# Kernel optimization log

Measured on AMD Instinct MI355X. Metric: run time of the kernel, lower is better.

Reference implementation:

```python
import jax, jax.numpy as jnp
import numpy as np

B, S, D = 4, 2048, 1024
H, HD = 16, 64
WINDOW = 128


def setup_inputs() -> dict:
    key = jax.random.key(0)
    ks = jax.random.split(key, 8)
    scale = 1.0 / np.sqrt(D)
    return {
        "hidden_states": jax.random.normal(ks[0], (B, S, D), dtype=jnp.float32),
        "attention_mask": jnp.zeros((B, 1, 1, S), dtype=jnp.float32),
        "Wq": jax.random.normal(ks[1], (D, D), dtype=jnp.float32) * scale,
        "bq": jnp.zeros((D,), dtype=jnp.float32),
        "Wk": jax.random.normal(ks[2], (D, D), dtype=jnp.float32) * scale,
        "bk": jnp.zeros((D,), dtype=jnp.float32),
        "Wv": jax.random.normal(ks[3], (D, D), dtype=jnp.float32) * scale,
        "bv": jnp.zeros((D,), dtype=jnp.float32),
    }


def _proj(x, W, b):
    # [b t D] -> [b h t d]
    p = x @ W.T + b
    return p.reshape(x.shape[0], x.shape[1], H, HD).transpose(0, 2, 1, 3)


def reference(hidden_states, attention_mask, Wq, bq, Wk, bk, Wv, bv):
    q = _proj(hidden_states, Wq, bq)  # [b h t d]
    k = _proj(hidden_states, Wk, bk)
    v = _proj(hidden_states, Wv, bv)

    scores = jnp.einsum("bhtd,bhsd->bhts", q, k) / np.sqrt(HD)  # [b h t s]
    pos = jnp.arange(S)
    i, j = pos[:, None], pos[None, :]
    # causal (j <= i) AND sliding window (i - j <= w)
    allowed = (j <= i) & ((i - j) <= WINDOW)  # [t s]
    scores = jnp.where(allowed[None, None], scores, -jnp.inf)
    scores = scores + attention_mask  # additive padding mask [b,1,1,s]
    probs = jax.nn.softmax(scores, axis=-1)  # dropout identity in eval
    ctx = jnp.einsum("bhts,bhsd->bhtd", probs, v)
    return ctx.transpose(0, 2, 1, 3).reshape(B, S, D)
```

## Files before the change

### kernel.cpp

```cpp
#include <hip/hip_runtime.h>
#include <cstdint>

#define BDIM 4
#define SEQ 2048
#define DMODEL 1024
#define NH 16
#define HDIM 64

typedef __attribute__((ext_vector_type(8))) short bf16x8;
typedef __attribute__((ext_vector_type(4))) float f32x4;
typedef __attribute__((ext_vector_type(4))) int i32x4;
typedef __attribute__((ext_vector_type(4))) unsigned short u16x4;

#define MFMA16(a, b, c) __builtin_amdgcn_mfma_f32_16x16x32_bf16(a, b, c, 0, 0, 0)

__device__ __forceinline__ unsigned short f2bf(float x) {
    unsigned int u = __float_as_uint(x);
    unsigned int r = (u + 0x7FFFu + ((u >> 16) & 1u)) >> 16;
    return (unsigned short)r;
}

__device__ __forceinline__ void gload16(const void* g, void* l) {
    __builtin_amdgcn_global_load_lds(
        (const __attribute__((address_space(1))) unsigned int*)g,
        (__attribute__((address_space(3))) unsigned int*)l, 16, 0, 0);
}

__global__ __launch_bounds__(256) void k_cvt_x(const float* __restrict__ src,
                                               unsigned short* __restrict__ dst) {
    int i = blockIdx.x * 256 + threadIdx.x;
    float4 v = ((const float4*)src)[i];
    u16x4 o = {f2bf(v.x), f2bf(v.y), f2bf(v.z), f2bf(v.w)};
    ((u16x4*)dst)[i] = o;
}

__global__ __launch_bounds__(256) void k_cvt_w(const float* __restrict__ wq,
                                               const float* __restrict__ wk,
                                               const float* __restrict__ wv,
                                               unsigned short* __restrict__ dst) {
    int i = blockIdx.x * 256 + threadIdx.x;
    int e = i << 2;
    int which = e >> 20;
    int off = e & 0xFFFFF;
    const float* s = which == 0 ? wq : (which == 1 ? wk : wv);
    float4 v = *(const float4*)(s + off);
    u16x4 o = {f2bf(v.x), f2bf(v.y), f2bf(v.z), f2bf(v.w)};
    ((u16x4*)dst)[i] = o;
}

__global__ __launch_bounds__(512, 2)
void k_qkv(const unsigned short* __restrict__ X,
           const unsigned short* __restrict__ W,
           const float* __restrict__ bq,
           const float* __restrict__ bk,
           const float* __restrict__ bv,
           unsigned short* __restrict__ Qo,
           unsigned short* __restrict__ Ko,
           unsigned short* __restrict__ Vt) {
    __shared__ unsigned short ldsA[2][2][256 * 32];
    __shared__ unsigned short ldsB[2][2][256 * 32];
    const int tid = threadIdx.x;
    const int lane = tid & 63, wid = tid >> 6;
    const int wm = wid >> 2, wn = wid & 3;
    const int l15 = lane & 15, g = lane >> 4;
    const int m0 = blockIdx.y * 256, n0 = blockIdx.x * 256;

#define STAGE_A(c, kk, kt)                                                        \
    {                                                                             \
        _Pragma("unroll") for (int i = 0; i < 2; ++i) {                           \
            const int e = i * 512 + tid;                                          \
            const int row = e >> 2, cc = e & 3;                                   \
            gload16(X + (size_t)(m0 + row) * DMODEL + (kt)*64 + (kk)*32 + cc * 8, \
                    (char*)&ldsA[c][kk][0] + e * 16);                             \
        }                                                                         \
    }
#define STAGE_B(c, kk, kt)                                                        \
    {                                                                             \
        _Pragma("unroll") for (int i = 0; i < 2; ++i) {                           \
            const int e = i * 512 + tid;                                          \
            const int row = e >> 2, cc = e & 3;                                   \
            gload16(W + (size_t)(n0 + row) * DMODEL + (kt)*64 + (kk)*32 + cc * 8, \
                    (char*)&ldsB[c][kk][0] + e * 16);                             \
        }                                                                         \
    }

    f32x4 acc[8][4];
#pragma unroll
    for (int i = 0; i < 8; ++i)
#pragma unroll
        for (int j = 0; j < 4; ++j) acc[i][j] = (f32x4){0.f, 0.f, 0.f, 0.f};

    STAGE_A(0, 0, 0); STAGE_B(0, 0, 0);
    STAGE_A(0, 1, 0); STAGE_B(0, 1, 0);
    STAGE_A(1, 0, 1); STAGE_B(1, 0, 1);
    asm volatile("s_waitcnt vmcnt(8)" ::: "memory");
    __builtin_amdgcn_s_barrier();

    const int arow = wm * 128 + l15;
    const int brow = wn * 64 + l15;

    for (int t = 0; t < 16; ++t) {
        const int c = t & 1;
        const char* Ab0 = (const char*)&ldsA[c][0][0];
        const char* Ab1 = (const char*)&ldsA[c][1][0];
        const char* Bb0 = (const char*)&ldsB[c][0][0];
        const char* Bb1 = (const char*)&ldsB[c][1][0];

        {
            bf16x8 av[8], bv0, bv1;
#pragma unroll
            for (int mf = 0; mf < 8; ++mf)
                av[mf] = *(const bf16x8*)(Ab0 + (arow + mf * 16) * 64 + g * 16);
            bv0 = *(const bf16x8*)(Bb0 + (brow) * 64 + g * 16);
            bv1 = *(const bf16x8*)(Bb0 + (brow + 16) * 64 + g * 16);
            if (t < 15) STAGE_A(c ^ 1, 1, t + 1);
            __builtin_amdgcn_s_barrier();
            asm volatile("s_waitcnt lgkmcnt(0)" ::: "memory");
            __builtin_amdgcn_sched_barrier(0);
            __builtin_amdgcn_s_setprio(1);
#pragma unroll
            for (int mf = 0; mf < 8; ++mf) {
                acc[mf][0] = MFMA16(av[mf], bv0, acc[mf][0]);
                acc[mf][1] = MFMA16(av[mf], bv1, acc[mf][1]);
            }
            __builtin_amdgcn_s_setprio(0);
            __builtin_amdgcn_s_barrier();

            bv0 = *(const bf16x8*)(Bb0 + (brow + 32) * 64 + g * 16);
            bv1 = *(const bf16x8*)(Bb0 + (brow + 48) * 64 + g * 16);
            if (t < 15) STAGE_B(c ^ 1, 1, t + 1);
            __builtin_amdgcn_s_barrier();
            asm volatile("s_waitcnt lgkmcnt(0)" ::: "memory");
            __builtin_amdgcn_sched_barrier(0);
            __builtin_amdgcn_s_setprio(1);
#pragma unroll
            for (int mf = 0; mf < 8; ++mf) {
                acc[mf][2] = MFMA16(av[mf], bv0, acc[mf][2]);
                acc[mf][3] = MFMA16(av[mf], bv1, acc[mf][3]);
            }
            __builtin_amdgcn_s_setprio(0);
            if (t < 15) { asm volatile("s_waitcnt vmcnt(8)" ::: "memory"); }
            else        { asm volatile("s_waitcnt vmcnt(0)" ::: "memory"); }
            __builtin_amdgcn_s_barrier();
        }

        {
            bf16x8 av[8], bv0, bv1;
#pragma unroll
            for (int mf = 0; mf < 8; ++mf)
                av[mf] = *(const bf16x8*)(Ab1 + (arow + mf * 16) * 64 + g * 16);
            bv0 = *(const bf16x8*)(Bb1 + (brow) * 64 + g * 16);
            bv1 = *(const bf16x8*)(Bb1 + (brow + 16) * 64 + g * 16);
            if (t < 14) STAGE_A(c, 0, t + 2);
            __builtin_amdgcn_s_barrier();
            asm volatile("s_waitcnt lgkmcnt(0)" ::: "memory");
            __builtin_amdgcn_sched_barrier(0);
            __builtin_amdgcn_s_setprio(1);
#pragma unroll
            for (int mf = 0; mf < 8; ++mf) {
                acc[mf][0] = MFMA16(av[mf], bv0, acc[mf][0]);
                acc[mf][1] = MFMA16(av[mf], bv1, acc[mf][1]);
            }
            __builtin_amdgcn_s_setprio(0);
            __builtin_amdgcn_s_barrier();

            bv0 = *(const bf16x8*)(Bb1 + (brow + 32) * 64 + g * 16);
            bv1 = *(const bf16x8*)(Bb1 + (brow + 48) * 64 + g * 16);
            if (t < 14) STAGE_B(c, 0, t + 2);
            __builtin_amdgcn_s_barrier();
            asm volatile("s_waitcnt lgkmcnt(0)" ::: "memory");
            __builtin_amdgcn_sched_barrier(0);
            __builtin_amdgcn_s_setprio(1);
#pragma unroll
            for (int mf = 0; mf < 8; ++mf) {
                acc[mf][2] = MFMA16(av[mf], bv0, acc[mf][2]);
                acc[mf][3] = MFMA16(av[mf], bv1, acc[mf][3]);
            }
            __builtin_amdgcn_s_setprio(0);
            if (t < 14)      { asm volatile("s_waitcnt vmcnt(8)" ::: "memory"); }
            else if (t == 14){ asm volatile("s_waitcnt vmcnt(4)" ::: "memory"); }
            __builtin_amdgcn_s_barrier();
        }
    }

    const int bb = m0 >> 11;
    const int sbase = (m0 & 2047) + wm * 128 + g * 4;
#pragma unroll
    for (int nf = 0; nf < 4; ++nf) {
        const int col = n0 + wn * 64 + nf * 16 + l15;
        const int proj = col >> 10, rem = col & 1023;
        const int h = rem >> 6, hd = rem & 63;
        const float bias = (proj == 0 ? bq : proj == 1 ? bk : bv)[rem];
        const float scl = (proj == 0) ? 0.125f : 1.0f;
        unsigned short* dstp = (proj == 0 ? Qo : proj == 1 ? Ko : Vt) +
                               (size_t)(bb * NH + h) * (SEQ * HDIM) +
                               (proj == 2 ? (size_t)hd * SEQ : (size_t)hd);
        const int stride = (proj == 2) ? 1 : HDIM;
#pragma unroll
        for (int mf = 0; mf < 8; ++mf) {
            const int s0 = sbase + mf * 16;
#pragma unroll
            for (int r = 0; r < 4; ++r)
                dstp[(size_t)(s0 + r) * stride] = f2bf((acc[mf][nf][r] + bias) * scl);
        }
    }
#undef STAGE_A
#undef STAGE_B
}

__global__ __launch_bounds__(256) void k_attn(const unsigned short* __restrict__ Qg,
                                              const unsigned short* __restrict__ Kg,
                                              const unsigned short* __restrict__ Vtg,
                                              const float* __restrict__ amask,
                                              float* __restrict__ out) {
    __shared__ unsigned short kl[224 * 64];
    __shared__ unsigned short vl[64 * 224];
    __shared__ unsigned short pl[4 * 16 * 160];
    const int bid0 = blockIdx.x;
    const int bid = (bid0 & 7) * 256 + (bid0 >> 3);
    const int bh = bid >> 5, qb = bid & 31;
    const int b = bh >> 4, h = bh & 15;
    const int q0 = qb << 6;
    const int kstart = q0 - 144;
    const int tid = threadIdx.x, lane = tid & 63, w = tid >> 6;
    const int l15 = lane & 15, g = lane >> 4;

#pragma unroll
    for (int it = 0; it < 7; ++it) {
        const int c = it * 256 + tid;
        {
            const int row = c >> 3, sl = c & 7;
            const int key = kstart + row;
            i32x4 v = {0, 0, 0, 0};
            if ((unsigned)key < (unsigned)SEQ)
                v = *(const i32x4*)(Kg + (size_t)(bh * SEQ + key) * HDIM + sl * 8);
            *(i32x4*)((char*)kl + ((row * 128 + sl * 16) ^ ((row & 7) << 4))) = v;
        }
        {
            const int row = c / 28, sl = c - row * 28;
            const int key0 = kstart + sl * 8;
            i32x4 v = {0, 0, 0, 0};
            if ((unsigned)key0 < (unsigned)SEQ)
                v = *(const i32x4*)(Vtg + (size_t)(bh * HDIM + row) * SEQ + key0);
            *(i32x4*)((char*)vl + ((row * 448 + sl * 16) ^ ((row & 7) << 4))) = v;
        }
    }
    const int iq = q0 + w * 16 + l15;
    const bf16x8 qf0 = *(const bf16x8*)(Qg + (size_t)(bh * SEQ + iq) * HDIM + g * 8);
    const bf16x8 qf1 = *(const bf16x8*)(Qg + (size_t)(bh * SEQ + iq) * HDIM + 32 + g * 8);
    __syncthreads();

    char* pbase = (char*)pl + w * 5120;
    const int swq = (l15 & 7) << 4;
    float s[40];

    __builtin_amdgcn_s_setprio(1);
#pragma unroll
    for (int t = 0; t < 5; ++t) {
        const int tloc = w * 16 + t * 32;
        bf16x8 kf[2][2];
#pragma unroll
        for (int m = 0; m < 2; ++m) {
            const int row = tloc + m * 16 + l15;
            const int swz = (row & 7) << 4;
            kf[m][0] = *(const bf16x8*)((const char*)kl + ((row * 128 + g * 16) ^ swz));
            kf[m][1] = *(const bf16x8*)((const char*)kl + ((row * 128 + 64 + g * 16) ^ swz));
        }
        f32x4 sa0 = {0.f, 0.f, 0.f, 0.f}, sa1 = {0.f, 0.f, 0.f, 0.f};
        sa0 = MFMA16(kf[0][0], qf0, sa0);
        sa0 = MFMA16(kf[0][1], qf1, sa0);
        sa1 = MFMA16(kf[1][0], qf0, sa1);
        sa1 = MFMA16(kf[1][1], qf1, sa1);
#pragma unroll
        for (int f = 0; f < 2; ++f) {
            const int jb = kstart + tloc + f * 16 + g * 4;
            float4 m4 = {0.f, 0.f, 0.f, 0.f};
            if ((unsigned)jb < (unsigned)SEQ) m4 = *(const float4*)(amask + b * SEQ + jb);
            const float mvv[4] = {m4.x, m4.y, m4.z, m4.w};
#pragma unroll
            for (int r = 0; r < 4; ++r) {
                const int jg = jb + r;
                const float sc = (f == 0 ? sa0[r] : sa1[r]) + mvv[r];
                const bool ok = (jg >= 0) && (jg <= iq) && (iq - jg <= 128);
                s[t * 8 + f * 4 + r] = ok ? sc : -3.0e38f;
            }
        }
    }
    __builtin_amdgcn_s_setprio(0);

    float tr[20];
#pragma unroll
    for (int i = 0; i < 20; ++i) tr[i] = fmaxf(s[i], s[i + 20]);
#pragma unroll
    for (int i = 0; i < 10; ++i) tr[i] = fmaxf(tr[i], tr[i + 10]);
#pragma unroll
    for (int i = 0; i < 5; ++i) tr[i] = fmaxf(tr[i], tr[i + 5]);
    float m = fmaxf(fmaxf(tr[0], tr[1]), fmaxf(tr[2], fmaxf(tr[3], tr[4])));
    m = fmaxf(m, __shfl_xor(m, 16));
    m = fmaxf(m, __shfl_xor(m, 32));

    float ls0 = 0.f, ls1 = 0.f, ls2 = 0.f, ls3 = 0.f;
#pragma unroll
    for (int i = 0; i < 40; i += 4) {
        float p0 = exp2f((s[i + 0] - m) * 1.44269504f);
        float p1 = exp2f((s[i + 1] - m) * 1.44269504f);
        float p2 = exp2f((s[i + 2] - m) * 1.44269504f);
        float p3 = exp2f((s[i + 3] - m) * 1.44269504f);
        s[i + 0] = p0; s[i + 1] = p1; s[i + 2] = p2; s[i + 3] = p3;
        ls0 += p0; ls1 += p1; ls2 += p2; ls3 += p3;
    }
    float l = (ls0 + ls1) + (ls2 + ls3);
    l += __shfl_xor(l, 16);
    l += __shfl_xor(l, 32);

#pragma unroll
    for (int t = 0; t < 5; ++t) {
#pragma unroll
        for (int f = 0; f < 2; ++f) {
            u16x4 pu = {f2bf(s[t * 8 + f * 4 + 0]), f2bf(s[t * 8 + f * 4 + 1]),
                        f2bf(s[t * 8 + f * 4 + 2]), f2bf(s[t * 8 + f * 4 + 3])};
            *(u16x4*)(pbase + ((l15 * 320 + t * 64 + f * 32 + g * 8) ^ swq)) = pu;
        }
    }
    asm volatile("s_waitcnt lgkmcnt(0)" ::: "memory");
    __builtin_amdgcn_sched_barrier(0);

    f32x4 acc[4];
#pragma unroll
    for (int i = 0; i < 4; ++i) acc[i] = (f32x4){0.f, 0.f, 0.f, 0.f};
    __builtin_amdgcn_s_setprio(1);
#pragma unroll
    for (int t = 0; t < 5; ++t) {
        const int tloc = w * 16 + t * 32;
        const bf16x8 pf = *(const bf16x8*)(pbase + ((l15 * 320 + t * 64 + g * 16) ^ swq));
#pragma unroll
        for (int fn = 0; fn < 4; ++fn) {
            const int vrow = fn * 16 + l15;
            const bf16x8 vf = *(const bf16x8*)((const char*)vl +
                ((vrow * 448 + tloc * 2 + g * 16) ^ ((vrow & 7) << 4)));
            acc[fn] = MFMA16(pf, vf, acc[fn]);
        }
    }
    __builtin_amdgcn_s_setprio(0);

    float linv[4];
#pragma unroll
    for (int r = 0; r < 4; ++r) linv[r] = 1.0f / __shfl(l, g * 4 + r);
#pragma unroll
    for (int fn = 0; fn < 4; ++fn) {
#pragma unroll
        for (int r = 0; r < 4; ++r) {
            const int qrow = q0 + w * 16 + g * 4 + r;
            out[(size_t)(b * SEQ + qrow) * DMODEL + h * HDIM + fn * 16 + l15] =
                acc[fn][r] * linv[r];
        }
    }
}

extern "C" void kernel_launch(void* const* d_in, const int* in_sizes, int n_in,
                              void* d_out, int out_size, void* d_ws, size_t ws_size,
                              hipStream_t stream) {
    const float* hs = (const float*)d_in[0];
    const float* amask = (const float*)d_in[1];
    const float* wq = (const float*)d_in[2];
    const float* bq = (const float*)d_in[3];
    const float* wk = (const float*)d_in[4];
    const float* bk = (const float*)d_in[5];
    const float* wv = (const float*)d_in[6];
    const float* bv = (const float*)d_in[7];
    float* out = (float*)d_out;

    char* p = (char*)d_ws;
    unsigned short* Xbf = (unsigned short*)p;
    unsigned short* Wbf = (unsigned short*)(p + 16777216);
    unsigned short* Vtb = (unsigned short*)(p + 16777216 + 6291456);
    unsigned short* Qb = Vtb + 8388608;
    unsigned short* Kb = Qb + 8388608;

    k_cvt_x<<<8192, 256, 0, stream>>>(hs, Xbf);
    k_cvt_w<<<3072, 256, 0, stream>>>(wq, wk, wv, Wbf);
    k_qkv<<<dim3(12, 32), 512, 0, stream>>>(Xbf, Wbf, bq, bk, bv, Qb, Kb, Vtb);
    k_attn<<<2048, 256, 0, stream>>>(Qb, Kb, Vtb, amask, out);
}
```

Baseline: 154.3 us.

## Swizzle GEMM LDS tiles, fuse convert kernels, transpose V in separate kernel

The two fp32-to-bf16 conversion kernels become one launch. The QKV GEMM's LDS tile layout gets an XOR swizzle on 16-byte chunks to avoid bank conflicts on fragment reads. V is now written row-major like Q and K instead of being scattered with stride-1-across-lanes transposed stores, and a new LDS-based transpose kernel produces Vt, reusing the X buffer. This trades an extra launch and an extra pass over V for coalesced GEMM epilogue writes.

```diff
diff --git a/kernel.cpp b/kernel.cpp
--- a/kernel.cpp
+++ b/kernel.cpp
@@ -26,26 +26,27 @@
         (__attribute__((address_space(3))) unsigned int*)l, 16, 0, 0);
 }
 
-__global__ __launch_bounds__(256) void k_cvt_x(const float* __restrict__ src,
-                                               unsigned short* __restrict__ dst) {
+__global__ __launch_bounds__(256) void k_cvt(const float* __restrict__ hs,
+                                             const float* __restrict__ wq,
+                                             const float* __restrict__ wk,
+                                             const float* __restrict__ wv,
+                                             unsigned short* __restrict__ Xbf,
+                                             unsigned short* __restrict__ Wbf) {
     int i = blockIdx.x * 256 + threadIdx.x;
-    float4 v = ((const float4*)src)[i];
-    u16x4 o = {f2bf(v.x), f2bf(v.y), f2bf(v.z), f2bf(v.w)};
-    ((u16x4*)dst)[i] = o;
-}
-
-__global__ __launch_bounds__(256) void k_cvt_w(const float* __restrict__ wq,
-                                               const float* __restrict__ wk,
-                                               const float* __restrict__ wv,
-                                               unsigned short* __restrict__ dst) {
-    int i = blockIdx.x * 256 + threadIdx.x;
-    int e = i << 2;
-    int which = e >> 20;
-    int off = e & 0xFFFFF;
-    const float* s = which == 0 ? wq : (which == 1 ? wk : wv);
-    float4 v = *(const float4*)(s + off);
-    u16x4 o = {f2bf(v.x), f2bf(v.y), f2bf(v.z), f2bf(v.w)};
-    ((u16x4*)dst)[i] = o;
+    if (i < 2097152) {
+        float4 v = ((const float4*)hs)[i];
+        u16x4 o = {f2bf(v.x), f2bf(v.y), f2bf(v.z), f2bf(v.w)};
+        ((u16x4*)Xbf)[i] = o;
+    } else {
+        int j = i - 2097152;
+        int e = j << 2;
+        int which = e >> 20;
+        int off = e & 0xFFFFF;
+        const float* s = which == 0 ? wq : (which == 1 ? wk : wv);
+        float4 v = *(const float4*)(s + off);
+        u16x4 o = {f2bf(v.x), f2bf(v.y), f2bf(v.z), f2bf(v.w)};
+        ((u16x4*)Wbf)[j] = o;
+    }
 }
 
 __global__ __launch_bounds__(512, 2)
@@ -56,7 +57,7 @@
            const float* __restrict__ bv,
            unsigned short* __restrict__ Qo,
            unsigned short* __restrict__ Ko,
-           unsigned short* __restrict__ Vt) {
+           unsigned short* __restrict__ Vo) {
     __shared__ unsigned short ldsA[2][2][256 * 32];
     __shared__ unsigned short ldsB[2][2][256 * 32];
     const int tid = threadIdx.x;
@@ -65,24 +66,28 @@
     const int l15 = lane & 15, g = lane >> 4;
     const int m0 = blockIdx.y * 256, n0 = blockIdx.x * 256;
 
-#define STAGE_A(c, kk, kt)                                                        \
-    {                                                                             \
-        _Pragma("unroll") for (int i = 0; i < 2; ++i) {                           \
-            const int e = i * 512 + tid;                                          \
-            const int row = e >> 2, cc = e & 3;                                   \
-            gload16(X + (size_t)(m0 + row) * DMODEL + (kt)*64 + (kk)*32 + cc * 8, \
-                    (char*)&ldsA[c][kk][0] + e * 16);                             \
-        }                                                                         \
-    }
-#define STAGE_B(c, kk, kt)                                                        \
-    {                                                                             \
-        _Pragma("unroll") for (int i = 0; i < 2; ++i) {                           \
-            const int e = i * 512 + tid;                                          \
-            const int row = e >> 2, cc = e & 3;                                   \
-            gload16(W + (size_t)(n0 + row) * DMODEL + (kt)*64 + (kk)*32 + cc * 8, \
-                    (char*)&ldsB[c][kk][0] + e * 16);                             \
-        }                                                                         \
-    }
+#define STAGE_A(c, kk, kt)                                                         \
+    {                                                                              \
+        _Pragma("unroll") for (int i = 0; i < 2; ++i) {                            \
+            const int e = i * 512 + tid;                                           \
+            const int row = e >> 2, cc = e & 3;                                    \
+            const int ccx = cc ^ ((row >> 1) & 3);                                 \
+            gload16(X + (size_t)(m0 + row) * DMODEL + (kt)*64 + (kk)*32 + ccx * 8, \
+                    (char*)&ldsA[c][kk][0] + e * 16);                              \
+        }                                                                          \
+    }
+#define STAGE_B(c, kk, kt)                                                         \
+    {                                                                              \
+        _Pragma("unroll") for (int i = 0; i < 2; ++i) {                            \
+            const int e = i * 512 + tid;                                           \
+            const int row = e >> 2, cc = e & 3;                                    \
+            const int ccx = cc ^ ((row >> 1) & 3);                                 \
+            gload16(W + (size_t)(n0 + row) * DMODEL + (kt)*64 + (kk)*32 + ccx * 8, \
+                    (char*)&ldsB[c][kk][0] + e * 16);                              \
+        }                                                                          \
+    }
+#define FRAG(base, row) \
+    (*(const bf16x8*)((const char*)(base) + (((row)*64 + g * 16) ^ ((((row) >> 1) & 3) << 4))))
 
     f32x4 acc[8][4];
 #pragma unroll
@@ -109,10 +114,9 @@
         {
             bf16x8 av[8], bv0, bv1;
 #pragma unroll
-            for (int mf = 0; mf < 8; ++mf)
-                av[mf] = *(const bf16x8*)(Ab0 + (arow + mf * 16) * 64 + g * 16);
-            bv0 = *(const bf16x8*)(Bb0 + (brow) * 64 + g * 16);
-            bv1 = *(const bf16x8*)(Bb0 + (brow + 16) * 64 + g * 16);
+            for (int mf = 0; mf < 8; ++mf) av[mf] = FRAG(Ab0, arow + mf * 16);
+            bv0 = FRAG(Bb0, brow);
+            bv1 = FRAG(Bb0, brow + 16);
             if (t < 15) STAGE_A(c ^ 1, 1, t + 1);
             __builtin_amdgcn_s_barrier();
             asm volatile("s_waitcnt lgkmcnt(0)" ::: "memory");
@@ -126,8 +130,8 @@
             __builtin_amdgcn_s_setprio(0);
             __builtin_amdgcn_s_barrier();
 
-            bv0 = *(const bf16x8*)(Bb0 + (brow + 32) * 64 + g * 16);
-            bv1 = *(const bf16x8*)(Bb0 + (brow + 48) * 64 + g * 16);
+            bv0 = FRAG(Bb0, brow + 32);
+            bv1 = FRAG(Bb0, brow + 48);
             if (t < 15) STAGE_B(c ^ 1, 1, t + 1);
             __builtin_amdgcn_s_barrier();
             asm volatile("s_waitcnt lgkmcnt(0)" ::: "memory");
@@ -147,10 +151,9 @@
         {
             bf16x8 av[8], bv0, bv1;
 #pragma unroll
-            for (int mf = 0; mf < 8; ++mf)
-                av[mf] = *(const bf16x8*)(Ab1 + (arow + mf * 16) * 64 + g * 16);
-            bv0 = *(const bf16x8*)(Bb1 + (brow) * 64 + g * 16);
-            bv1 = *(const bf16x8*)(Bb1 + (brow + 16) * 64 + g * 16);
+            for (int mf = 0; mf < 8; ++mf) av[mf] = FRAG(Ab1, arow + mf * 16);
+            bv0 = FRAG(Bb1, brow);
+            bv1 = FRAG(Bb1, brow + 16);
             if (t < 14) STAGE_A(c, 0, t + 2);
             __builtin_amdgcn_s_barrier();
             asm volatile("s_waitcnt lgkmcnt(0)" ::: "memory");
@@ -164,8 +167,8 @@
             __builtin_amdgcn_s_setprio(0);
             __builtin_amdgcn_s_barrier();
 
-            bv0 = *(const bf16x8*)(Bb1 + (brow + 32) * 64 + g * 16);
-            bv1 = *(const bf16x8*)(Bb1 + (brow + 48) * 64 + g * 16);
+            bv0 = FRAG(Bb1, brow + 32);
+            bv1 = FRAG(Bb1, brow + 48);
             if (t < 14) STAGE_B(c, 0, t + 2);
             __builtin_amdgcn_s_barrier();
             asm volatile("s_waitcnt lgkmcnt(0)" ::: "memory");
@@ -183,29 +186,54 @@
         }
     }
 
-    const int bb = m0 >> 11;
-    const int sbase = (m0 & 2047) + wm * 128 + g * 4;
 #pragma unroll
     for (int nf = 0; nf < 4; ++nf) {
         const int col = n0 + wn * 64 + nf * 16 + l15;
         const int proj = col >> 10, rem = col & 1023;
         const int h = rem >> 6, hd = rem & 63;
-        const float bias = (proj == 0 ? bq : proj == 1 ? bk : bv)[rem];
+        const float* bp = proj == 0 ? bq : (proj == 1 ? bk : bv);
+        const float bias = bp[rem];
         const float scl = (proj == 0) ? 0.125f : 1.0f;
-        unsigned short* dstp = (proj == 0 ? Qo : proj == 1 ? Ko : Vt) +
-                               (size_t)(bb * NH + h) * (SEQ * HDIM) +
-                               (proj == 2 ? (size_t)hd * SEQ : (size_t)hd);
-        const int stride = (proj == 2) ? 1 : HDIM;
+        unsigned short* dst = proj == 0 ? Qo : (proj == 1 ? Ko : Vo);
 #pragma unroll
         for (int mf = 0; mf < 8; ++mf) {
-            const int s0 = sbase + mf * 16;
-#pragma unroll
-            for (int r = 0; r < 4; ++r)
-                dstp[(size_t)(s0 + r) * stride] = f2bf((acc[mf][nf][r] + bias) * scl);
+#pragma unroll
+            for (int r = 0; r < 4; ++r) {
+                const int m = m0 + wm * 128 + mf * 16 + g * 4 + r;
+                const int bb = m >> 11, s = m & 2047;
+                dst[(size_t)((bb * NH + h) * SEQ + s) * HDIM + hd] =
+                    f2bf((acc[mf][nf][r] + bias) * scl);
+            }
         }
     }
 #undef STAGE_A
 #undef STAGE_B
+#undef FRAG
+}
+
+__global__ __launch_bounds__(256) void k_trv(const unsigned short* __restrict__ V,
+                                             unsigned short* __restrict__ Vt) {
+    __shared__ unsigned short tl[64][80];
+    const int bh = blockIdx.y, s0 = blockIdx.x * 64;
+    const int tid = threadIdx.x;
+#pragma unroll
+    for (int it = 0; it < 2; ++it) {
+        const int c = it * 256 + tid;
+        const int sl = c >> 3, hs = c & 7;
+        i32x4 v = *(const i32x4*)(V + (size_t)(bh * SEQ + s0 + sl) * HDIM + hs * 8);
+        union { i32x4 v; unsigned short u[8]; } uu;
+        uu.v = v;
+#pragma unroll
+        for (int j = 0; j < 8; ++j) tl[hs * 8 + j][sl] = uu.u[j];
+    }
+    __syncthreads();
+#pragma unroll
+    for (int it = 0; it < 2; ++it) {
+        const int c = it * 256 + tid;
+        const int hd = c >> 3, ss = c & 7;
+        i32x4 o = *(const i32x4*)(&tl[hd][ss * 8]);
+        *(i32x4*)(Vt + (size_t)(bh * HDIM + hd) * SEQ + s0 + ss * 8) = o;
+    }
 }
 
 __global__ __launch_bounds__(256) void k_attn(const unsigned short* __restrict__ Qg,
@@ -373,12 +401,13 @@
     char* p = (char*)d_ws;
     unsigned short* Xbf = (unsigned short*)p;
     unsigned short* Wbf = (unsigned short*)(p + 16777216);
-    unsigned short* Vtb = (unsigned short*)(p + 16777216 + 6291456);
-    unsigned short* Qb = Vtb + 8388608;
+    unsigned short* Qb = (unsigned short*)(p + 16777216 + 6291456);
     unsigned short* Kb = Qb + 8388608;
-
-    k_cvt_x<<<8192, 256, 0, stream>>>(hs, Xbf);
-    k_cvt_w<<<3072, 256, 0, stream>>>(wq, wk, wv, Wbf);
-    k_qkv<<<dim3(12, 32), 512, 0, stream>>>(Xbf, Wbf, bq, bk, bv, Qb, Kb, Vtb);
+    unsigned short* Vb = Kb + 8388608;
+    unsigned short* Vtb = Xbf;
+
+    k_cvt<<<11264, 256, 0, stream>>>(hs, wq, wk, wv, Xbf, Wbf);
+    k_qkv<<<dim3(12, 32), 512, 0, stream>>>(Xbf, Wbf, bq, bk, bv, Qb, Kb, Vb);
+    k_trv<<<dim3(32, 64), 256, 0, stream>>>(Vb, Vtb);
     k_attn<<<2048, 256, 0, stream>>>(Qb, Kb, Vtb, amask, out);
 }
```

New measurement: 136.8 us. -11.3%, faster.
